# Performance work log

Hardware: AMD Instinct MI355X
Metric: run time of the kernel (lower is better)

The kernel has to match this reference:

```python
import jax, jax.numpy as jnp
import numpy as np
from jax import lax

D_MODEL = 768
CHUNK = 128
LR = 0.01
MOMENTUM_DECAY = 0.9
FORGET_GATE = 0.01


def setup_inputs() -> dict:
    key = jax.random.key(0)
    ks = jax.random.split(key, 6)
    return {
        "W": jax.random.normal(ks[0], (D_MODEL, D_MODEL), jnp.float32) * 0.02,
        "b_param": jax.random.normal(ks[1], (D_MODEL,), jnp.float32) * 0.02,
        "keys": jax.random.normal(ks[2], (CHUNK, D_MODEL), jnp.float32),
        "values": jax.random.normal(ks[3], (CHUNK, D_MODEL), jnp.float32),
        "momentum_W": jax.random.normal(ks[4], (D_MODEL, D_MODEL), jnp.float32) * 0.01,
        "momentum_b": jax.random.normal(ks[5], (D_MODEL,), jnp.float32) * 0.01,
    }


def _scan_last(eta, inputs):
    """Associative scan S_t = eta*S_{t-1} + inputs_t; returns full sequence.

    inputs: (T, D). eta is a scalar gate (constant across t, matching the
    original module which builds a full (T,) eta vector of one value).
    """
    T = inputs.shape[0]
    a = jnp.full((T, 1), eta, dtype=inputs.dtype)

    def combine(c1, c2):
        a1, b1 = c1
        a2, b2 = c2
        return (a1 * a2, a2 * b1 + b2)

    _, seq = lax.associative_scan(combine, (a, inputs))
    return seq


def reference(W, b_param, keys, values, momentum_W, momentum_b):
    T = keys.shape[0]
    W0 = lax.stop_gradient(W)          # .detach() in torch
    b0 = lax.stop_gradient(b_param)

    # predictions (T, d_out) = (W0 @ keys.T).T
    preds_lin = keys @ W0.T
    err_W = preds_lin - values                      # used for W grads (no bias)
    # per-token outer-product gradients: (T, d_out, d_in)
    W_grads = 2.0 * err_W[:, :, None] * keys[:, None, :]

    preds = preds_lin + b0
    err_b = preds - values
    b_grads = 2.0 * err_b
    losses = jnp.mean(err_b ** 2, axis=1)

    alphas = jnp.full((T,), FORGET_GATE, dtype=keys.dtype)
    betas = jnp.exp(jnp.cumsum(jnp.log1p(-alphas)))          # cumulative decay
    beta_ratios = betas[-1] / jnp.clip(betas, 1e-10)
    thetas = jnp.full((T,), LR, dtype=keys.dtype)
    scale = thetas * beta_ratios                              # (T,)

    # --- W momentum scan over flattened state (T, d_out*d_in) ---
    scaled_W_grads = scale[:, None, None] * W_grads
    W_inputs = -scaled_W_grads.reshape(T, -1)
    W_inputs = W_inputs.at[0].add(MOMENTUM_DECAY * momentum_W.reshape(-1))
    W_seq = _scan_last(MOMENTUM_DECAY, W_inputs)
    new_momentum_W = W_seq[-1].reshape(W.shape)

    # --- bias momentum scan (T, d_out) ---
    b_inputs = -(scale[:, None] * b_grads)
    b_inputs = b_inputs.at[0].add(MOMENTUM_DECAY * momentum_b)
    b_seq = _scan_last(MOMENTUM_DECAY, b_inputs)
    new_momentum_b = b_seq[-1]

    beta_total = betas[-1]
    W_new = beta_total * W0 + new_momentum_W
    b_new = beta_total * b0 + new_momentum_b
    return (W_new, b_new, new_momentum_W, new_momentum_b, losses)
```

## Files before the change

### kernel.cpp

```cpp
#include <hip/hip_runtime.h>
#include <math.h>

#define D 768
#define T 128
#define KC 16
#define CHUNKK (D / KC)
#define NSUB (CHUNKK / 16)

#define LN_ETA_DECAY (-0.11541085151132775f)

__global__ __launch_bounds__(512) void k1_pgemm(
    const float* __restrict__ W,
    const float* __restrict__ keys,
    float* __restrict__ Ppart,
    float* __restrict__ losses)
{
    __shared__ float sKt[16][132];
    __shared__ float sWo[16][68];

    const int obase = blockIdx.x * 64;
    const int kbase = blockIdx.y * CHUNKK;
    const int tid = threadIdx.x;
    const int ty = tid >> 4;
    const int tx = tid & 15;
    const int t0 = tid >> 2;
    const int q0 = tid & 3;
    const int o0 = (tid >> 2) & 63;

    if (blockIdx.x == 0 && blockIdx.y == 0 && tid < T) losses[tid] = 0.f;

    float acc[4][4];
    #pragma unroll
    for (int j = 0; j < 4; ++j)
        #pragma unroll
        for (int n = 0; n < 4; ++n) acc[j][n] = 0.f;

    float4 gk = *reinterpret_cast<const float4*>(keys + t0 * D + kbase + q0 * 4);
    float4 gw;
    if (tid < 256)
        gw = *reinterpret_cast<const float4*>(W + (obase + o0) * D + kbase + q0 * 4);

    for (int c = 0; c < NSUB; ++c) {
        sKt[q0 * 4 + 0][t0] = gk.x;
        sKt[q0 * 4 + 1][t0] = gk.y;
        sKt[q0 * 4 + 2][t0] = gk.z;
        sKt[q0 * 4 + 3][t0] = gk.w;
        if (tid < 256) {
            sWo[q0 * 4 + 0][o0] = gw.x;
            sWo[q0 * 4 + 1][o0] = gw.y;
            sWo[q0 * 4 + 2][o0] = gw.z;
            sWo[q0 * 4 + 3][o0] = gw.w;
        }
        __syncthreads();

        if (c + 1 < NSUB) {
            const int kb = kbase + (c + 1) * 16;
            gk = *reinterpret_cast<const float4*>(keys + t0 * D + kb + q0 * 4);
            if (tid < 256)
                gw = *reinterpret_cast<const float4*>(W + (obase + o0) * D + kb + q0 * 4);
        }

        #pragma unroll
        for (int k = 0; k < 16; ++k) {
            float4 a = *reinterpret_cast<const float4*>(&sKt[k][ty * 4]);
            float4 b = *reinterpret_cast<const float4*>(&sWo[k][tx * 4]);
            const float av[4] = { a.x, a.y, a.z, a.w };
            const float bv[4] = { b.x, b.y, b.z, b.w };
            #pragma unroll
            for (int j = 0; j < 4; ++j)
                #pragma unroll
                for (int n = 0; n < 4; ++n) acc[j][n] += av[j] * bv[n];
        }
        __syncthreads();
    }

    float* outp = Ppart + blockIdx.y * (T * D);
    #pragma unroll
    for (int j = 0; j < 4; ++j) {
        const int t = ty * 4 + j;
        float4 v = { acc[j][0], acc[j][1], acc[j][2], acc[j][3] };
        *reinterpret_cast<float4*>(outp + t * D + obase + tx * 4) = v;
    }
}

__global__ __launch_bounds__(256) void k15_reduce(
    const float* __restrict__ Ppart,
    const float* __restrict__ values,
    float* __restrict__ errW)
{
    const int off = (blockIdx.x * 256 + threadIdx.x) * 2;
    float2 vv = *reinterpret_cast<const float2*>(values + off);
    float2 s = { -vv.x, -vv.y };
    #pragma unroll
    for (int kc = 0; kc < KC; ++kc) {
        float2 v = *reinterpret_cast<const float2*>(Ppart + kc * (T * D) + off);
        s.x += v.x; s.y += v.y;
    }
    *reinterpret_cast<float2*>(errW + off) = s;
}

__global__ __launch_bounds__(256) void k2_main(
    const float* __restrict__ errW,
    const float* __restrict__ keys,
    const float* __restrict__ W,
    const float* __restrict__ mW,
    const float* __restrict__ bparam,
    const float* __restrict__ mb,
    float* __restrict__ W_new,
    float* __restrict__ b_new,
    float* __restrict__ mW_new,
    float* __restrict__ mb_new,
    float* __restrict__ losses,
    float pow_eta_T, float beta_total, float Csum)
{
    __shared__ float sErr[T][64];
    __shared__ float sKs[T][64];
    __shared__ float sC[T];
    __shared__ float sB0[64];

    const int oT = blockIdx.x / 12, iT = blockIdx.x % 12;
    const int obase = oT * 64, ibase = iT * 64;
    const int tid = threadIdx.x;
    const int ty = tid >> 4, tx = tid & 15;

    float4 pm[4], pw[4];
    #pragma unroll
    for (int aa = 0; aa < 4; ++aa) {
        const int o = obase + ty * 4 + aa;
        const int i = ibase + tx * 4;
        pm[aa] = *reinterpret_cast<const float4*>(mW + o * D + i);
        pw[aa] = *reinterpret_cast<const float4*>(W + o * D + i);
    }

    if (tid < T)  sC[tid]  = 0.01f * __expf((float)(127 - tid) * LN_ETA_DECAY);
    if (tid < 64) sB0[tid] = bparam[obase + tid];

    #pragma unroll
    for (int p = 0; p < 8; ++p) {
        const int idx = tid + p * 256;
        const int t = idx >> 4, q = idx & 15;
        float4 ev = *reinterpret_cast<const float4*>(errW + t * D + obase + q * 4);
        *reinterpret_cast<float4*>(&sErr[t][q * 4]) = ev;

        const float c2 = 2.f * 0.01f * __expf((float)(127 - t) * LN_ETA_DECAY);
        float4 kv = *reinterpret_cast<const float4*>(keys + t * D + ibase + q * 4);
        kv.x *= c2; kv.y *= c2; kv.z *= c2; kv.w *= c2;
        *reinterpret_cast<float4*>(&sKs[t][q * 4]) = kv;
    }
    __syncthreads();

    float acc[4][4];
    #pragma unroll
    for (int a = 0; a < 4; ++a)
        #pragma unroll
        for (int b = 0; b < 4; ++b) acc[a][b] = 0.f;

    #pragma unroll 4
    for (int t = 0; t < T; ++t) {
        float4 a = *reinterpret_cast<const float4*>(&sErr[t][ty * 4]);
        float4 b = *reinterpret_cast<const float4*>(&sKs[t][tx * 4]);
        const float av[4] = { a.x, a.y, a.z, a.w };
        const float bv[4] = { b.x, b.y, b.z, b.w };
        #pragma unroll
        for (int aa = 0; aa < 4; ++aa)
            #pragma unroll
            for (int bb = 0; bb < 4; ++bb) acc[aa][bb] += av[aa] * bv[bb];
    }

    #pragma unroll
    for (int aa = 0; aa < 4; ++aa) {
        const int o = obase + ty * 4 + aa;
        const int i = ibase + tx * 4;
        float4 nm, wn;
        nm.x = pow_eta_T * pm[aa].x - acc[aa][0];
        nm.y = pow_eta_T * pm[aa].y - acc[aa][1];
        nm.z = pow_eta_T * pm[aa].z - acc[aa][2];
        nm.w = pow_eta_T * pm[aa].w - acc[aa][3];
        wn.x = beta_total * pw[aa].x + nm.x;
        wn.y = beta_total * pw[aa].y + nm.y;
        wn.z = beta_total * pw[aa].z + nm.z;
        wn.w = beta_total * pw[aa].w + nm.w;
        *reinterpret_cast<float4*>(mW_new + o * D + i) = nm;
        *reinterpret_cast<float4*>(W_new + o * D + i) = wn;
    }

    if (iT == 0 && tid < 64) {
        float S = 0.f;
        for (int t = 0; t < T; ++t) S += sC[t] * sErr[t][tid];
        const int o = obase + tid;
        const float nmb = pow_eta_T * mb[o] - 2.f * S - 2.f * Csum * sB0[tid];
        mb_new[o] = nmb;
        b_new[o]  = beta_total * sB0[tid] + nmb;
    }

    if (iT == 1) {
        const int t = tid >> 1, h = tid & 1;
        float L = 0.f;
        #pragma unroll 8
        for (int oo = 0; oo < 32; ++oo) {
            const int o = ((h * 32 + oo) + t) & 63;
            const float e = sErr[t][o] + sB0[o];
            L += e * e;
        }
        L += __shfl_xor(L, 1, 64);
        if (h == 0) atomicAdd(losses + t, L * (1.f / 768.f));
    }
}

extern "C" void kernel_launch(void* const* d_in, const int* in_sizes, int n_in,
                              void* d_out, int out_size, void* d_ws, size_t ws_size,
                              hipStream_t stream) {
    const float* W      = (const float*)d_in[0];
    const float* bparam = (const float*)d_in[1];
    const float* keys   = (const float*)d_in[2];
    const float* values = (const float*)d_in[3];
    const float* mW     = (const float*)d_in[4];
    const float* mb     = (const float*)d_in[5];

    float* out = (float*)d_out;
    float* W_new  = out;
    float* b_new  = out + 589824;
    float* mW_new = out + 590592;
    float* mb_new = out + 1180416;
    float* losses = out + 1181184;

    float* Ppart = (float*)d_ws;
    float* errW  = Ppart + KC * T * D;

    double cs = 0.0;
    for (int t = 0; t < T; ++t) cs += 0.01 * pow(0.891, 127 - t);
    const float pow_eta_T  = (float)pow(0.9, 128);
    const float beta_total = (float)pow(0.99, 128);
    const float Csum = (float)cs;

    k1_pgemm<<<dim3(12, KC), 512, 0, stream>>>(W, keys, Ppart, losses);
    k15_reduce<<<192, 256, 0, stream>>>(Ppart, values, errW);
    k2_main<<<144, 256, 0, stream>>>(errW, keys, W, mW, bparam, mb,
                                     W_new, b_new, mW_new, mb_new, losses,
                                     pow_eta_T, beta_total, Csum);
}
```

Measured before the change: 84.07 us.

## Fuse split-K partial reduction into main kernel with blocked Ppart layout

Removes the separate reduce kernel. The main kernel now sums the 16 split-K partial products plus -values directly into shared memory as the error tile. Ppart is re-laid out per output tile (contiguous 128x64 blocks) so each main block reads its slice contiguously. The main kernel grows to 512 threads so the extra loads spread across more threads, while only 256 threads run the outer-product GEMM. The cost is redundant reads: each of the 12 i-tile blocks sharing an o-tile re-reads and re-reduces the same 16 partials.

```diff
diff --git a/kernel.cpp b/kernel.cpp
--- a/kernel.cpp
+++ b/kernel.cpp
@@ -18,8 +18,10 @@
     __shared__ float sKt[16][132];
     __shared__ float sWo[16][68];
 
-    const int obase = blockIdx.x * 64;
-    const int kbase = blockIdx.y * CHUNKK;
+    const int bx = blockIdx.x;
+    const int by = blockIdx.y;
+    const int obase = bx * 64;
+    const int kbase = by * CHUNKK;
     const int tid = threadIdx.x;
     const int ty = tid >> 4;
     const int tx = tid & 15;
@@ -27,7 +29,7 @@
     const int q0 = tid & 3;
     const int o0 = (tid >> 2) & 63;
 
-    if (blockIdx.x == 0 && blockIdx.y == 0 && tid < T) losses[tid] = 0.f;
+    if (bx == 0 && by == 0 && tid < T) losses[tid] = 0.f;
 
     float acc[4][4];
     #pragma unroll
@@ -74,33 +76,18 @@
         __syncthreads();
     }
 
-    float* outp = Ppart + blockIdx.y * (T * D);
+    float* outp = Ppart + (bx * KC + by) * (T * 64);
     #pragma unroll
     for (int j = 0; j < 4; ++j) {
         const int t = ty * 4 + j;
         float4 v = { acc[j][0], acc[j][1], acc[j][2], acc[j][3] };
-        *reinterpret_cast<float4*>(outp + t * D + obase + tx * 4) = v;
+        *reinterpret_cast<float4*>(outp + t * 64 + tx * 4) = v;
     }
 }
 
-__global__ __launch_bounds__(256) void k15_reduce(
+__global__ __launch_bounds__(512) void k2_main(
     const float* __restrict__ Ppart,
     const float* __restrict__ values,
-    float* __restrict__ errW)
-{
-    const int off = (blockIdx.x * 256 + threadIdx.x) * 2;
-    float2 vv = *reinterpret_cast<const float2*>(values + off);
-    float2 s = { -vv.x, -vv.y };
-    #pragma unroll
-    for (int kc = 0; kc < KC; ++kc) {
-        float2 v = *reinterpret_cast<const float2*>(Ppart + kc * (T * D) + off);
-        s.x += v.x; s.y += v.y;
-    }
-    *reinterpret_cast<float2*>(errW + off) = s;
-}
-
-__global__ __launch_bounds__(256) void k2_main(
-    const float* __restrict__ errW,
     const float* __restrict__ keys,
     const float* __restrict__ W,
     const float* __restrict__ mW,
@@ -124,64 +111,80 @@
     const int ty = tid >> 4, tx = tid & 15;
 
     float4 pm[4], pw[4];
-    #pragma unroll
-    for (int aa = 0; aa < 4; ++aa) {
-        const int o = obase + ty * 4 + aa;
-        const int i = ibase + tx * 4;
-        pm[aa] = *reinterpret_cast<const float4*>(mW + o * D + i);
-        pw[aa] = *reinterpret_cast<const float4*>(W + o * D + i);
+    if (tid < 256) {
+        #pragma unroll
+        for (int aa = 0; aa < 4; ++aa) {
+            const int o = obase + ty * 4 + aa;
+            const int i = ibase + tx * 4;
+            pm[aa] = *reinterpret_cast<const float4*>(mW + o * D + i);
+            pw[aa] = *reinterpret_cast<const float4*>(W + o * D + i);
+        }
     }
 
     if (tid < T)  sC[tid]  = 0.01f * __expf((float)(127 - tid) * LN_ETA_DECAY);
     if (tid < 64) sB0[tid] = bparam[obase + tid];
 
     #pragma unroll
-    for (int p = 0; p < 8; ++p) {
-        const int idx = tid + p * 256;
+    for (int r = 0; r < 4; ++r) {
+        const int idx = tid + r * 512;
         const int t = idx >> 4, q = idx & 15;
-        float4 ev = *reinterpret_cast<const float4*>(errW + t * D + obase + q * 4);
-        *reinterpret_cast<float4*>(&sErr[t][q * 4]) = ev;
-
         const float c2 = 2.f * 0.01f * __expf((float)(127 - t) * LN_ETA_DECAY);
         float4 kv = *reinterpret_cast<const float4*>(keys + t * D + ibase + q * 4);
         kv.x *= c2; kv.y *= c2; kv.z *= c2; kv.w *= c2;
         *reinterpret_cast<float4*>(&sKs[t][q * 4]) = kv;
     }
+
+    const float* Pp = Ppart + oT * (KC * T * 64);
+    #pragma unroll
+    for (int r = 0; r < 4; ++r) {
+        const int idx = tid + r * 512;
+        const int t = idx >> 4, q = idx & 15;
+        float4 vv = *reinterpret_cast<const float4*>(values + t * D + obase + q * 4);
+        float4 s = { -vv.x, -vv.y, -vv.z, -vv.w };
+        #pragma unroll
+        for (int kc = 0; kc < KC; ++kc) {
+            float4 v = *reinterpret_cast<const float4*>(Pp + kc * (T * 64) + t * 64 + q * 4);
+            s.x += v.x; s.y += v.y; s.z += v.z; s.w += v.w;
+        }
+        *reinterpret_cast<float4*>(&sErr[t][q * 4]) = s;
+    }
     __syncthreads();
 
-    float acc[4][4];
-    #pragma unroll
-    for (int a = 0; a < 4; ++a)
-        #pragma unroll
-        for (int b = 0; b < 4; ++b) acc[a][b] = 0.f;
-
-    #pragma unroll 4
-    for (int t = 0; t < T; ++t) {
-        float4 a = *reinterpret_cast<const float4*>(&sErr[t][ty * 4]);
-        float4 b = *reinterpret_cast<const float4*>(&sKs[t][tx * 4]);
-        const float av[4] = { a.x, a.y, a.z, a.w };
-        const float bv[4] = { b.x, b.y, b.z, b.w };
-        #pragma unroll
-        for (int aa = 0; aa < 4; ++aa)
+    if (tid < 256) {
+        float acc[4][4];
+        #pragma unroll
+        for (int a = 0; a < 4; ++a)
             #pragma unroll
-            for (int bb = 0; bb < 4; ++bb) acc[aa][bb] += av[aa] * bv[bb];
-    }
-
-    #pragma unroll
-    for (int aa = 0; aa < 4; ++aa) {
-        const int o = obase + ty * 4 + aa;
-        const int i = ibase + tx * 4;
-        float4 nm, wn;
-        nm.x = pow_eta_T * pm[aa].x - acc[aa][0];
-        nm.y = pow_eta_T * pm[aa].y - acc[aa][1];
-        nm.z = pow_eta_T * pm[aa].z - acc[aa][2];
-        nm.w = pow_eta_T * pm[aa].w - acc[aa][3];
-        wn.x = beta_total * pw[aa].x + nm.x;
-        wn.y = beta_total * pw[aa].y + nm.y;
-        wn.z = beta_total * pw[aa].z + nm.z;
-        wn.w = beta_total * pw[aa].w + nm.w;
-        *reinterpret_cast<float4*>(mW_new + o * D + i) = nm;
-        *reinterpret_cast<float4*>(W_new + o * D + i) = wn;
+            for (int n = 0; n < 4; ++n) acc[a][n] = 0.f;
+
+        #pragma unroll 4
+        for (int t = 0; t < T; ++t) {
+            float4 a = *reinterpret_cast<const float4*>(&sErr[t][ty * 4]);
+            float4 b = *reinterpret_cast<const float4*>(&sKs[t][tx * 4]);
+            const float av[4] = { a.x, a.y, a.z, a.w };
+            const float bv[4] = { b.x, b.y, b.z, b.w };
+            #pragma unroll
+            for (int aa = 0; aa < 4; ++aa)
+                #pragma unroll
+                for (int bb = 0; bb < 4; ++bb) acc[aa][bb] += av[aa] * bv[bb];
+        }
+
+        #pragma unroll
+        for (int aa = 0; aa < 4; ++aa) {
+            const int o = obase + ty * 4 + aa;
+            const int i = ibase + tx * 4;
+            float4 nm, wn;
+            nm.x = pow_eta_T * pm[aa].x - acc[aa][0];
+            nm.y = pow_eta_T * pm[aa].y - acc[aa][1];
+            nm.z = pow_eta_T * pm[aa].z - acc[aa][2];
+            nm.w = pow_eta_T * pm[aa].w - acc[aa][3];
+            wn.x = beta_total * pw[aa].x + nm.x;
+            wn.y = beta_total * pw[aa].y + nm.y;
+            wn.z = beta_total * pw[aa].z + nm.z;
+            wn.w = beta_total * pw[aa].w + nm.w;
+            *reinterpret_cast<float4*>(mW_new + o * D + i) = nm;
+            *reinterpret_cast<float4*>(W_new + o * D + i) = wn;
+        }
     }
 
     if (iT == 0 && tid < 64) {
@@ -193,7 +196,7 @@
         b_new[o]  = beta_total * sB0[tid] + nmb;
     }
 
-    if (iT == 1) {
+    if (iT == 1 && tid < 256) {
         const int t = tid >> 1, h = tid & 1;
         float L = 0.f;
         #pragma unroll 8
@@ -225,7 +228,6 @@
     float* losses = out + 1181184;
 
     float* Ppart = (float*)d_ws;
-    float* errW  = Ppart + KC * T * D;
 
     double cs = 0.0;
     for (int t = 0; t < T; ++t) cs += 0.01 * pow(0.891, 127 - t);
@@ -234,8 +236,7 @@
     const float Csum = (float)cs;
 
     k1_pgemm<<<dim3(12, KC), 512, 0, stream>>>(W, keys, Ppart, losses);
-    k15_reduce<<<192, 256, 0, stream>>>(Ppart, values, errW);
-    k2_main<<<144, 256, 0, stream>>>(errW, keys, W, mW, bparam, mb,
+    k2_main<<<144, 512, 0, stream>>>(Ppart, values, keys, W, mW, bparam, mb,
                                      W_new, b_new, mW_new, mb_new, losses,
                                      pow_eta_T, beta_total, Csum);
 }
```

Result: slower. 93.42 us (+11.1%).
